# Kernel tuning notes

Measured on AMD Instinct MI355X. Metric: run time of the kernel, lower is better.

The kernel has to match this reference:

```python
import jax, jax.numpy as jnp
import numpy as np

ALPHA = 0.2          # LeakyReLU negative slope
NEG_BIG = -9e15      # mask value from original code


def setup_inputs() -> dict:
    key = jax.random.key(0)
    k1, k2, k3, k4 = jax.random.split(key, 4)
    B, N, F_in, F_out = 16, 1024, 256, 256
    x = jax.random.normal(k1, (B, N, F_in), dtype=jnp.float32)
    adj = jax.random.randint(k2, (B, N, N), 0, 2, dtype=jnp.int32)
    # xavier-uniform-like scales
    W = jax.random.normal(k3, (F_in, F_out), dtype=jnp.float32) * np.sqrt(2.0 / (F_in + F_out))
    a = jax.random.normal(k4, (2 * F_out, 1), dtype=jnp.float32) * np.sqrt(2.0 / (2 * F_out + 1))
    return {"x": x, "adj": adj, "W": W, "a": a}


def reference(x, adj, W, a):
    # x: [B,N,Fin], adj: [B,N,N] (int mask), W: [Fin,Fout], a: [2*Fout,1]
    F_out = a.shape[0] // 2
    h = jnp.einsum("bni,io->bno", x, W)            # [B,N,Fout]
    # Decompose a into left/right halves: e_ij = lrelu(a_l.h_i + a_r.h_j)
    a_l = a[:F_out, 0]                               # [Fout]
    a_r = a[F_out:, 0]                               # [Fout]
    el = h @ a_l                                     # [B,N] score contribution of target i
    er = h @ a_r                                     # [B,N] score contribution of source j
    e = jax.nn.leaky_relu(el[:, :, None] + er[:, None, :], ALPHA)  # [B,N,N]
    e = jnp.where(adj > 0, e, NEG_BIG)
    attn = jax.nn.softmax(e, axis=-1)                # masked softmax over neighbors j
    # weighted sum of neighbor features; concat with n_heads=1 is identity
    return jnp.einsum("bij,bjo->bio", attn, h)       # [B,N,Fout]
```

## Files before the change

kernel.cpp:

```cpp
#include <hip/hip_runtime.h>
#include <stdint.h>

#define ALPHA 0.2f
#define NEG_BIG -9000000000000000.0f
#define L2E 1.4426950408889634f

typedef __attribute__((ext_vector_type(8))) short bf16x8;
typedef __attribute__((ext_vector_type(8))) unsigned short u16x8;
typedef __attribute__((ext_vector_type(4))) float f32x4;

__device__ __forceinline__ unsigned short f2bf(float f) {
    unsigned int u = __float_as_uint(f);
    u += 0x7fffu + ((u >> 16) & 1u);
    return (unsigned short)(u >> 16);
}

__device__ __forceinline__ void gload_lds16(const void* g, void* l) {
    __builtin_amdgcn_global_load_lds(
        (const __attribute__((address_space(1))) unsigned int*)g,
        (__attribute__((address_space(3))) unsigned int*)l, 16, 0, 0);
}

__global__ void wt_wa_kernel(const float* __restrict__ W,
                             const float* __restrict__ a,
                             unsigned short* __restrict__ Wtbf,
                             float* __restrict__ wa) {
    const int t = threadIdx.x;
    if (blockIdx.x < 256) {
        const int o = blockIdx.x;
        Wtbf[o * 256 + t] = f2bf(W[t * 256 + o]);
    } else {
        float sl = 0.f, sr = 0.f;
        const float* wr = W + t * 256;
        for (int o = 0; o < 256; ++o) {
            const float wv = wr[o];
            sl += wv * a[o];
            sr += wv * a[256 + o];
        }
        wa[t] = sl;
        wa[256 + t] = sr;
    }
}

__global__ __launch_bounds__(256) void eler2x_kernel(
    const float* __restrict__ x, const float* __restrict__ wa,
    float* __restrict__ el, float* __restrict__ er,
    unsigned short* __restrict__ xbf)
{
    const int w = threadIdx.x >> 6, l = threadIdx.x & 63;
    const int r = blockIdx.x * 4 + w;
    const float4 xv = *(const float4*)(x + (size_t)r * 256 + l * 4);
    const float4 al = *(const float4*)(wa + l * 4);
    const float4 ar = *(const float4*)(wa + 256 + l * 4);

    ushort4 xb;
    xb.x = f2bf(xv.x); xb.y = f2bf(xv.y); xb.z = f2bf(xv.z); xb.w = f2bf(xv.w);
    *(ushort4*)(xbf + (size_t)r * 256 + l * 4) = xb;

    float sl = xv.x * al.x + xv.y * al.y + xv.z * al.z + xv.w * al.w;
    float sr = xv.x * ar.x + xv.y * ar.y + xv.z * ar.z + xv.w * ar.w;
#pragma unroll
    for (int off = 32; off >= 1; off >>= 1) {
        sl += __shfl_xor(sl, off);
        sr += __shfl_xor(sr, off);
    }
    if (l == 0) { el[r] = sl * L2E; er[r] = sr * L2E; }
}

__global__ __launch_bounds__(256) void gemm_h(
    const unsigned short* __restrict__ A,
    const unsigned short* __restrict__ Bt,
    unsigned short* __restrict__ C)
{
    __shared__ __align__(16) unsigned short As[2 * 64 * 64];
    __shared__ __align__(16) unsigned short Bs[2 * 128 * 64];

    const int tid = threadIdx.x;
    const int w = tid >> 6, l = tid & 63;
    const int q = l >> 4, ml = l & 15;
    const int wm = (w >> 1) * 32;
    const int wn = (w & 1) * 64;
    const int m0 = blockIdx.y * 64;
    const int n0 = blockIdx.x * 128;

    f32x4 acc[2][4];
#pragma unroll
    for (int i = 0; i < 2; ++i)
#pragma unroll
        for (int j = 0; j < 4; ++j) {
            f32x4 z = {0.f, 0.f, 0.f, 0.f};
            acc[i][j] = z;
        }

#define GSTAGE(BI, K0) do {                                                   \
    _Pragma("unroll")                                                         \
    for (int c_ = 0; c_ < 2; ++c_) {                                          \
        const int cb_ = c_ * 256 + (w << 6);                                  \
        const int p_ = cb_ + l;                                               \
        const int r_ = p_ >> 3;                                               \
        const int cc_ = (p_ & 7) ^ (r_ & 7);                                  \
        gload_lds16(A + (size_t)(m0 + r_) * 256 + (K0) + cc_ * 8,             \
                    As + (BI) * 4096 + cb_ * 8);                              \
    }                                                                         \
    _Pragma("unroll")                                                         \
    for (int c_ = 0; c_ < 4; ++c_) {                                          \
        const int cb_ = c_ * 256 + (w << 6);                                  \
        const int p_ = cb_ + l;                                               \
        const int r_ = p_ >> 3;                                               \
        const int cc_ = (p_ & 7) ^ (r_ & 7);                                  \
        gload_lds16(Bt + (size_t)(n0 + r_) * 256 + (K0) + cc_ * 8,            \
                    Bs + (BI) * 8192 + cb_ * 8);                              \
    } } while (0)

    GSTAGE(0, 0);

    for (int s = 0; s < 4; ++s) {
        const int cur = s & 1;
        if (s + 1 < 4) {
            GSTAGE((s + 1) & 1, (s + 1) * 64);
            asm volatile("s_waitcnt vmcnt(6) lgkmcnt(0)" ::: "memory");
        } else {
            asm volatile("s_waitcnt vmcnt(0) lgkmcnt(0)" ::: "memory");
        }
        __builtin_amdgcn_s_barrier();
        __builtin_amdgcn_sched_barrier(0);

        const unsigned short* Ab = As + cur * 4096;
        const unsigned short* Bb = Bs + cur * 8192;
        bf16x8 aF[2][2], bF[2][4];
#pragma unroll
        for (int ks = 0; ks < 2; ++ks) {
#pragma unroll
            for (int mt = 0; mt < 2; ++mt) {
                const int mm = wm + mt * 16 + ml;
                aF[ks][mt] = *(const bf16x8*)(Ab + (mm * 8 + ((ks * 4 + q) ^ (mm & 7))) * 8);
            }
#pragma unroll
            for (int nt = 0; nt < 4; ++nt) {
                const int nn = wn + nt * 16 + ml;
                bF[ks][nt] = *(const bf16x8*)(Bb + (nn * 8 + ((ks * 4 + q) ^ (nn & 7))) * 8);
            }
        }
#pragma unroll
        for (int ks = 0; ks < 2; ++ks)
            for (int mt = 0; mt < 2; ++mt)
                for (int nt = 0; nt < 4; ++nt)
                    acc[mt][nt] = __builtin_amdgcn_mfma_f32_16x16x32_bf16(
                        aF[ks][mt], bF[ks][nt], acc[mt][nt], 0, 0, 0);

        asm volatile("s_waitcnt lgkmcnt(0)" ::: "memory");
        __builtin_amdgcn_s_barrier();
    }
#undef GSTAGE

    for (int mt = 0; mt < 2; ++mt)
        for (int nt = 0; nt < 4; ++nt) {
            const int gn = n0 + wn + nt * 16 + ml;
            for (int r = 0; r < 4; ++r) {
                const int gm = m0 + wm + mt * 16 + q * 4 + r;
                C[(size_t)gm * 16384 + gn] = f2bf(acc[mt][nt][r]);
            }
        }
}

__global__ __launch_bounds__(256) void mask_kernel(
    const int* __restrict__ adj,
    const float* __restrict__ el,
    const float* __restrict__ er,
    float* __restrict__ c,
    unsigned short* __restrict__ pk16)
{
    __shared__ unsigned char nibs[4][256];

    const int w = threadIdx.x >> 6, l = threadIdx.x & 63;
    const int row = blockIdx.x * 4 + w;
    const int b = row >> 10;
    const int* arow = adj + (size_t)row * 1024;
    const float* erb = er + (b << 10);
    const float eli = el[row];

    float ev[16];
    float m = -3.0e38f;
#pragma unroll
    for (int it = 0; it < 4; ++it) {
        const int j = it * 256 + l * 4;
        const int4 av = *(const int4*)(arow + j);
        const float4 erv = *(const float4*)(erb + j);
        float e0 = eli + erv.x; e0 = e0 > 0.f ? e0 : ALPHA * e0; e0 = av.x > 0 ? e0 : NEG_BIG;
        float e1 = eli + erv.y; e1 = e1 > 0.f ? e1 : ALPHA * e1; e1 = av.y > 0 ? e1 : NEG_BIG;
        float e2 = eli + erv.z; e2 = e2 > 0.f ? e2 : ALPHA * e2; e2 = av.z > 0 ? e2 : NEG_BIG;
        float e3 = eli + erv.w; e3 = e3 > 0.f ? e3 : ALPHA * e3; e3 = av.w > 0 ? e3 : NEG_BIG;
        ev[it * 4 + 0] = e0; ev[it * 4 + 1] = e1;
        ev[it * 4 + 2] = e2; ev[it * 4 + 3] = e3;
        m = fmaxf(m, fmaxf(fmaxf(e0, e1), fmaxf(e2, e3)));
        nibs[w][it * 64 + l] =
            (unsigned char)((av.x > 0) | ((av.y > 0) << 1) |
                            ((av.z > 0) << 2) | ((av.w > 0) << 3));
    }
#pragma unroll
    for (int off = 32; off >= 1; off >>= 1) m = fmaxf(m, __shfl_xor(m, off));
    float s = 0.f;
#pragma unroll
    for (int u = 0; u < 16; ++u) s += exp2f(ev[u] - m);
#pragma unroll
    for (int off = 32; off >= 1; off >>= 1) s += __shfl_xor(s, off);
    if (l == 0) c[row] = m + log2f(s);

    const unsigned nr = *(const unsigned int*)(&nibs[w][l * 4]);
    const unsigned short mask16 =
        (unsigned short)((nr & 0xFu) | ((nr >> 4) & 0xF0u) |
                         ((nr >> 8) & 0xF00u) | ((nr >> 12) & 0xF000u));
    pk16[(size_t)row * 64 + l] = mask16;
}

__global__ __launch_bounds__(512) void pv_kernel(
    const unsigned short* __restrict__ pk16,
    const float* __restrict__ el2,
    const float* __restrict__ er2,
    const float* __restrict__ c2,
    const unsigned short* __restrict__ hT,
    float* __restrict__ out)
{
    __shared__ float er_s[1024];
    __shared__ __align__(16) unsigned short pk_s[64 * 64];
    __shared__ __align__(16) unsigned short Hs[2 * 256 * 32];
    __shared__ __align__(16) unsigned short Ps[2 * 64 * 40];

    const int tid = threadIdx.x;
    const int w = tid >> 6, l = tid & 63;
    const int q = l >> 4, ml = l & 15;
    const int wm = (w >> 2) * 32;
    const int wn = (w & 3) * 64;

    const int bid = blockIdx.x;
    const int slot = bid >> 3;
    const int b = ((bid & 7) << 1) | (slot >> 4);
    const int i0 = (slot & 15) * 64;

    *(float2*)(er_s + tid * 2) = *(const float2*)(er2 + (b << 10) + tid * 2);
    *(u16x8*)(pk_s + (tid >> 3) * 64 + (tid & 7) * 8) =
        *(const u16x8*)(pk16 + (size_t)((b << 10) + i0 + (tid >> 3)) * 64 + (tid & 7) * 8);

    const int ib = tid >> 3;
    const int js = (tid & 7) * 4;
    const int rg = (b << 10) + i0 + ib;
    const float el2i = el2[rg];
    const float c2i = c2[rg];

    f32x4 acc[2][4];
#pragma unroll
    for (int i = 0; i < 2; ++i)
#pragma unroll
        for (int j = 0; j < 4; ++j) {
            f32x4 z = {0.f, 0.f, 0.f, 0.f};
            acc[i][j] = z;
        }

    const unsigned short* hb = hT + (size_t)b * 1024;

#define STAGE(BI, T) do {                                                     \
    const int jb_ = (T) * 32;                                                 \
    _Pragma("unroll")                                                         \
    for (int c_ = 0; c_ < 2; ++c_) {                                          \
        const int cb_ = c_ * 512 + (w << 6);                                  \
        const int p_ = cb_ + l;                                               \
        const int r_ = p_ >> 2;                                               \
        const int cc_ = (p_ & 3) ^ ((r_ >> 1) & 3);                           \
        gload_lds16(hb + (size_t)r_ * 16384 + jb_ + cc_ * 8,                  \
                    Hs + (BI) * 8192 + cb_ * 8);                              \
    } } while (0)

#define BUILD(BI, T) do {                                                     \
    const int jb_ = (T) * 32;                                                 \
    const float4 ev_ = *(const float4*)(er_s + jb_ + js);                     \
    const unsigned hw_ = pk_s[ib * 64 + ((jb_ + js) >> 4)];                   \
    const unsigned mv_ = (hw_ >> (js & 12)) & 0xFu;                           \
    float e0_ = el2i + ev_.x; e0_ = fmaxf(e0_, ALPHA * e0_);                  \
    float e1_ = el2i + ev_.y; e1_ = fmaxf(e1_, ALPHA * e1_);                  \
    float e2_ = el2i + ev_.z; e2_ = fmaxf(e2_, ALPHA * e2_);                  \
    float e3_ = el2i + ev_.w; e3_ = fmaxf(e3_, ALPHA * e3_);                  \
    ushort4 pv_;                                                              \
    pv_.x = (mv_ & 1u) ? f2bf(exp2f(e0_ - c2i)) : (unsigned short)0;          \
    pv_.y = (mv_ & 2u) ? f2bf(exp2f(e1_ - c2i)) : (unsigned short)0;          \
    pv_.z = (mv_ & 4u) ? f2bf(exp2f(e2_ - c2i)) : (unsigned short)0;          \
    pv_.w = (mv_ & 8u) ? f2bf(exp2f(e3_ - c2i)) : (unsigned short)0;          \
    *(ushort4*)(Ps + (BI) * 2560 + ib * 40 + js) = pv_;                       \
    } while (0)

#define COMPUTE(BI) do {                                                      \
    bf16x8 aF_[2], bF_[4];                                                    \
    _Pragma("unroll")                                                         \
    for (int mt_ = 0; mt_ < 2; ++mt_)                                         \
        aF_[mt_] = *(const bf16x8*)(Ps + (BI) * 2560 +                        \
                                    (wm + mt_ * 16 + ml) * 40 + q * 8);       \
    _Pragma("unroll")                                                         \
    for (int nt_ = 0; nt_ < 4; ++nt_) {                                       \
        const int oc_ = wn + nt_ * 16 + ml;                                   \
        const int sl_ = q ^ ((oc_ >> 1) & 3);                                 \
        bF_[nt_] = *(const bf16x8*)(Hs + (BI) * 8192 + oc_ * 32 + sl_ * 8);   \
    }                                                                         \
    _Pragma("unroll")                                                         \
    for (int mt_ = 0; mt_ < 2; ++mt_)                                         \
        _Pragma("unroll")                                                     \
        for (int nt_ = 0; nt_ < 4; ++nt_)                                     \
            acc[mt_][nt_] = __builtin_amdgcn_mfma_f32_16x16x32_bf16(          \
                aF_[mt_], bF_[nt_], acc[mt_][nt_], 0, 0, 0);                  \
    } while (0)

    STAGE(0, 0);
    asm volatile("s_waitcnt lgkmcnt(0)" ::: "memory");
    __builtin_amdgcn_s_barrier();

    for (int t = 0; t < 32; ++t) {
        const int cur = t & 1;
        if (t + 1 < 32) STAGE((t + 1) & 1, t + 1);
        BUILD(cur, t);
        if (t + 1 < 32)
            asm volatile("s_waitcnt vmcnt(2) lgkmcnt(0)" ::: "memory");
        else
            asm volatile("s_waitcnt vmcnt(0) lgkmcnt(0)" ::: "memory");
        __builtin_amdgcn_s_barrier();
        __builtin_amdgcn_sched_barrier(0);
        COMPUTE(cur);
        asm volatile("s_waitcnt lgkmcnt(0)" ::: "memory");
        __builtin_amdgcn_s_barrier();
    }

#undef STAGE
#undef BUILD
#undef COMPUTE

    float* ob = out + (size_t)b * 262144;
#pragma unroll
    for (int mt = 0; mt < 2; ++mt)
#pragma unroll
        for (int nt = 0; nt < 4; ++nt) {
            const int gn = wn + nt * 16 + ml;
#pragma unroll
            for (int r = 0; r < 4; ++r) {
                const int gm = i0 + wm + mt * 16 + q * 4 + r;
                ob[(size_t)gm * 256 + gn] = acc[mt][nt][r];
            }
        }
}

extern "C" void kernel_launch(void* const* d_in, const int* in_sizes, int n_in,
                              void* d_out, int out_size, void* d_ws, size_t ws_size,
                              hipStream_t stream) {
    const float* x   = (const float*)d_in[0];
    const int*   adj = (const int*)d_in[1];
    const float* W   = (const float*)d_in[2];
    const float* a   = (const float*)d_in[3];
    float* out = (float*)d_out;

    char* ws = (char*)d_ws;
    unsigned short* Wtbf  = (unsigned short*)(ws);
    float* wa             = (float*)(ws + 131072);
    unsigned short* xbf   = (unsigned short*)(ws + 133120);
    unsigned short* h_T   = (unsigned short*)(ws + 8521728);
    float* el             = (float*)(ws + 16910336);
    float* er             = (float*)(ws + 16975872);
    float* c              = (float*)(ws + 17041408);
    unsigned short* pk16  = (unsigned short*)(ws + 17106944);

    wt_wa_kernel<<<dim3(257), dim3(256), 0, stream>>>(W, a, Wtbf, wa);

    eler2x_kernel<<<dim3(4096), dim3(256), 0, stream>>>(x, wa, el, er, xbf);

    gemm_h<<<dim3(128, 4), dim3(256), 0, stream>>>(Wtbf, xbf, h_T);

    mask_kernel<<<dim3(4096), dim3(256), 0, stream>>>(adj, el, er, c, pk16);

    pv_kernel<<<dim3(256), dim3(512), 0, stream>>>(pk16, el, er, c, h_T, out);
}
```

Measured before the change: 157.9 us.

## Fuse mask/softmax-stats kernel into PV kernel with online softmax in registers

Measured after the change: 169.6 us. 7.4% more time.

```diff
diff --git a/kernel.cpp b/kernel.cpp
--- a/kernel.cpp
+++ b/kernel.cpp
@@ -163,66 +163,15 @@
         }
 }
 
-__global__ __launch_bounds__(256) void mask_kernel(
+__global__ __launch_bounds__(512) void maskpv_kernel(
     const int* __restrict__ adj,
-    const float* __restrict__ el,
-    const float* __restrict__ er,
-    float* __restrict__ c,
-    unsigned short* __restrict__ pk16)
-{
-    __shared__ unsigned char nibs[4][256];
-
-    const int w = threadIdx.x >> 6, l = threadIdx.x & 63;
-    const int row = blockIdx.x * 4 + w;
-    const int b = row >> 10;
-    const int* arow = adj + (size_t)row * 1024;
-    const float* erb = er + (b << 10);
-    const float eli = el[row];
-
-    float ev[16];
-    float m = -3.0e38f;
-#pragma unroll
-    for (int it = 0; it < 4; ++it) {
-        const int j = it * 256 + l * 4;
-        const int4 av = *(const int4*)(arow + j);
-        const float4 erv = *(const float4*)(erb + j);
-        float e0 = eli + erv.x; e0 = e0 > 0.f ? e0 : ALPHA * e0; e0 = av.x > 0 ? e0 : NEG_BIG;
-        float e1 = eli + erv.y; e1 = e1 > 0.f ? e1 : ALPHA * e1; e1 = av.y > 0 ? e1 : NEG_BIG;
-        float e2 = eli + erv.z; e2 = e2 > 0.f ? e2 : ALPHA * e2; e2 = av.z > 0 ? e2 : NEG_BIG;
-        float e3 = eli + erv.w; e3 = e3 > 0.f ? e3 : ALPHA * e3; e3 = av.w > 0 ? e3 : NEG_BIG;
-        ev[it * 4 + 0] = e0; ev[it * 4 + 1] = e1;
-        ev[it * 4 + 2] = e2; ev[it * 4 + 3] = e3;
-        m = fmaxf(m, fmaxf(fmaxf(e0, e1), fmaxf(e2, e3)));
-        nibs[w][it * 64 + l] =
-            (unsigned char)((av.x > 0) | ((av.y > 0) << 1) |
-                            ((av.z > 0) << 2) | ((av.w > 0) << 3));
-    }
-#pragma unroll
-    for (int off = 32; off >= 1; off >>= 1) m = fmaxf(m, __shfl_xor(m, off));
-    float s = 0.f;
-#pragma unroll
-    for (int u = 0; u < 16; ++u) s += exp2f(ev[u] - m);
-#pragma unroll
-    for (int off = 32; off >= 1; off >>= 1) s += __shfl_xor(s, off);
-    if (l == 0) c[row] = m + log2f(s);
-
-    const unsigned nr = *(const unsigned int*)(&nibs[w][l * 4]);
-    const unsigned short mask16 =
-        (unsigned short)((nr & 0xFu) | ((nr >> 4) & 0xF0u) |
-                         ((nr >> 8) & 0xF00u) | ((nr >> 12) & 0xF000u));
-    pk16[(size_t)row * 64 + l] = mask16;
-}
-
-__global__ __launch_bounds__(512) void pv_kernel(
-    const unsigned short* __restrict__ pk16,
     const float* __restrict__ el2,
     const float* __restrict__ er2,
-    const float* __restrict__ c2,
     const unsigned short* __restrict__ hT,
     float* __restrict__ out)
 {
     __shared__ float er_s[1024];
-    __shared__ __align__(16) unsigned short pk_s[64 * 64];
+    __shared__ float c_s[64];
     __shared__ __align__(16) unsigned short Hs[2 * 256 * 32];
     __shared__ __align__(16) unsigned short Ps[2 * 64 * 40];
 
@@ -237,15 +186,71 @@
     const int b = ((bid & 7) << 1) | (slot >> 4);
     const int i0 = (slot & 15) * 64;
 
-    *(float2*)(er_s + tid * 2) = *(const float2*)(er2 + (b << 10) + tid * 2);
-    *(u16x8*)(pk_s + (tid >> 3) * 64 + (tid & 7) * 8) =
-        *(const u16x8*)(pk16 + (size_t)((b << 10) + i0 + (tid >> 3)) * 64 + (tid & 7) * 8);
-
     const int ib = tid >> 3;
     const int js = (tid & 7) * 4;
     const int rg = (b << 10) + i0 + ib;
     const float el2i = el2[rg];
-    const float c2i = c2[rg];
+
+    const unsigned short* hb = hT + (size_t)b * 1024;
+
+#define STAGE(BI, T) do {                                                     \
+    const int jb_ = (T) * 32;                                                 \
+    _Pragma("unroll")                                                         \
+    for (int c_ = 0; c_ < 2; ++c_) {                                          \
+        const int cb_ = c_ * 512 + tid;                                       \
+        const int r_ = cb_ >> 2;                                              \
+        const int cc_ = (cb_ & 3) ^ ((r_ >> 1) & 3);                          \
+        gload_lds16(hb + (size_t)r_ * 16384 + jb_ + cc_ * 8,                  \
+                    Hs + (BI) * 8192 + (cb_ << 3));                           \
+    } } while (0)
+
+    STAGE(0, 0);
+
+    *(float2*)(er_s + tid * 2) = *(const float2*)(er2 + (b << 10) + tid * 2);
+    asm volatile("s_waitcnt lgkmcnt(0)" ::: "memory");
+    __builtin_amdgcn_s_barrier();
+
+    unsigned mw[4];
+    float m1 = -3.0e38f, s1 = 0.f;
+    const int* arow = adj + (size_t)rg * 1024 + js;
+#pragma unroll
+    for (int kw = 0; kw < 4; ++kw) {
+        unsigned wbits = 0;
+#pragma unroll
+        for (int j = 0; j < 8; ++j) {
+            const int k = kw * 8 + j;
+            const int4 av = *(const int4*)(arow + k * 32);
+            const float4 erv = *(const float4*)(er_s + js + k * 32);
+            float e0 = el2i + erv.x; e0 = fmaxf(e0, ALPHA * e0);
+            float e1 = el2i + erv.y; e1 = fmaxf(e1, ALPHA * e1);
+            float e2 = el2i + erv.z; e2 = fmaxf(e2, ALPHA * e2);
+            float e3 = el2i + erv.w; e3 = fmaxf(e3, ALPHA * e3);
+            e0 = av.x > 0 ? e0 : -3.0e38f;
+            e1 = av.y > 0 ? e1 : -3.0e38f;
+            e2 = av.z > 0 ? e2 : -3.0e38f;
+            e3 = av.w > 0 ? e3 : -3.0e38f;
+            wbits |= ((av.x > 0 ? 1u : 0u) | (av.y > 0 ? 2u : 0u) |
+                      (av.z > 0 ? 4u : 0u) | (av.w > 0 ? 8u : 0u)) << (j * 4);
+            const float mc = fmaxf(fmaxf(e0, e1), fmaxf(e2, e3));
+            const float nm = fmaxf(m1, mc);
+            s1 = s1 * exp2f(m1 - nm) + exp2f(e0 - nm) + exp2f(e1 - nm)
+               + exp2f(e2 - nm) + exp2f(e3 - nm);
+            m1 = nm;
+        }
+        mw[kw] = wbits;
+    }
+#pragma unroll
+    for (int off = 1; off <= 4; off <<= 1) {
+        const float mo = __shfl_xor(m1, off);
+        const float so = __shfl_xor(s1, off);
+        const float nm = fmaxf(m1, mo);
+        s1 = s1 * exp2f(m1 - nm) + so * exp2f(mo - nm);
+        m1 = nm;
+    }
+    if ((tid & 7) == 0) c_s[ib] = m1 + log2f(s1);
+    asm volatile("s_waitcnt lgkmcnt(0)" ::: "memory");
+    __builtin_amdgcn_s_barrier();
+    const float c2i = c_s[ib];
 
     f32x4 acc[2][4];
 #pragma unroll
@@ -256,25 +261,10 @@
             acc[i][j] = z;
         }
 
-    const unsigned short* hb = hT + (size_t)b * 1024;
-
-#define STAGE(BI, T) do {                                                     \
-    const int jb_ = (T) * 32;                                                 \
-    _Pragma("unroll")                                                         \
-    for (int c_ = 0; c_ < 2; ++c_) {                                          \
-        const int cb_ = c_ * 512 + (w << 6);                                  \
-        const int p_ = cb_ + l;                                               \
-        const int r_ = p_ >> 2;                                               \
-        const int cc_ = (p_ & 3) ^ ((r_ >> 1) & 3);                           \
-        gload_lds16(hb + (size_t)r_ * 16384 + jb_ + cc_ * 8,                  \
-                    Hs + (BI) * 8192 + cb_ * 8);                              \
-    } } while (0)
-
-#define BUILD(BI, T) do {                                                     \
+#define BUILDR(BI, T) do {                                                    \
     const int jb_ = (T) * 32;                                                 \
     const float4 ev_ = *(const float4*)(er_s + jb_ + js);                     \
-    const unsigned hw_ = pk_s[ib * 64 + ((jb_ + js) >> 4)];                   \
-    const unsigned mv_ = (hw_ >> (js & 12)) & 0xFu;                           \
+    const unsigned mv_ = (mw[(T) >> 3] >> (((T) & 7) * 4)) & 0xFu;            \
     float e0_ = el2i + ev_.x; e0_ = fmaxf(e0_, ALPHA * e0_);                  \
     float e1_ = el2i + ev_.y; e1_ = fmaxf(e1_, ALPHA * e1_);                  \
     float e2_ = el2i + ev_.z; e2_ = fmaxf(e2_, ALPHA * e2_);                  \
@@ -307,14 +297,11 @@
                 aF_[mt_], bF_[nt_], acc[mt_][nt_], 0, 0, 0);                  \
     } while (0)
 
-    STAGE(0, 0);
-    asm volatile("s_waitcnt lgkmcnt(0)" ::: "memory");
-    __builtin_amdgcn_s_barrier();
-
+#pragma unroll
     for (int t = 0; t < 32; ++t) {
         const int cur = t & 1;
         if (t + 1 < 32) STAGE((t + 1) & 1, t + 1);
-        BUILD(cur, t);
+        BUILDR(cur, t);
         if (t + 1 < 32)
             asm volatile("s_waitcnt vmcnt(2) lgkmcnt(0)" ::: "memory");
         else
@@ -327,7 +314,7 @@
     }
 
 #undef STAGE
-#undef BUILD
+#undef BUILDR
 #undef COMPUTE
 
     float* ob = out + (size_t)b * 262144;
@@ -360,8 +347,6 @@
     unsigned short* h_T   = (unsigned short*)(ws + 8521728);
     float* el             = (float*)(ws + 16910336);
     float* er             = (float*)(ws + 16975872);
-    float* c              = (float*)(ws + 17041408);
-    unsigned short* pk16  = (unsigned short*)(ws + 17106944);
 
     wt_wa_kernel<<<dim3(257), dim3(256), 0, stream>>>(W, a, Wtbf, wa);
 
@@ -369,7 +354,5 @@
 
     gemm_h<<<dim3(128, 4), dim3(256), 0, stream>>>(Wtbf, xbf, h_T);
 
-    mask_kernel<<<dim3(4096), dim3(256), 0, stream>>>(adj, el, er, c, pk16);
-
-    pv_kernel<<<dim3(256), dim3(512), 0, stream>>>(pk16, el, er, c, h_T, out);
-}
+    maskpv_kernel<<<dim3(256), dim3(512), 0, stream>>>(adj, el, er, h_T, out);
+}
```
